# Kernel optimization log

Hardware: AMD Instinct MI355X
Metric: run time of the kernel (lower is better)

Reference implementation:

```python
import jax, jax.numpy as jnp
import numpy as np

B, T, HID = 1, 1024, 2048
H, DK, DV, M, KW = 16, 128, 128, 128, 4  # heads, key dim, value dim, slots, conv kernel
SCALE = DK ** -0.5
EPS = 1e-5


def short_conv(x, w):
    # causal depthwise conv1d + silu; x: [B,T,C], w: [C,K]
    K = w.shape[1]
    xp = jnp.pad(x, ((0, 0), (K - 1, 0), (0, 0)))
    t = x.shape[1]
    y = sum(xp[:, i:i + t] * w[:, i] for i in range(K))
    return jax.nn.silu(y)


def l2norm(x):
    return x * jax.lax.rsqrt(jnp.sum(x * x, axis=-1, keepdims=True) + 1e-6)


def gsa2_scan(q, k, v, w, g, beta):
    # q,k: [B,T,H,DK]  v: [B,T,H,DV]  w,g: [B,T,H,M]  beta: [B,T,H]
    b = q.shape[0]
    tm = lambda x: jnp.moveaxis(x, 1, 0)  # time-major
    Sk0 = jnp.zeros((b, H, DK, M), q.dtype)  # key->slot memory
    Sv0 = jnp.zeros((b, H, M, DV), q.dtype)  # slot->value memory

    def step(carry, xs):
        Sk, Sv = carry
        q_t, k_t, v_t, w_t, g_t, b_t = xs
        gt = jnp.exp(g_t)  # [B,H,M] gate in (0,1) since g = logsigmoid(.)
        bw = b_t[:, :, None] * w_t  # beta-scaled slot write address [B,H,M]
        Sk = Sk * gt[:, :, None, :] + k_t[..., :, None] * bw[:, :, None, :]
        Sv = Sv * gt[..., None] + bw[..., None] * v_t[:, :, None, :]
        s = jnp.einsum('bhd,bhdm->bhm', q_t, Sk) * SCALE
        a = jax.nn.softmax(s, axis=-1)
        o_t = jnp.einsum('bhm,bhmd->bhd', a, Sv)
        return (Sk, Sv), o_t

    (_, _), o = jax.lax.scan(step, (Sk0, Sv0),
                             (tm(q), tm(k), tm(v), tm(w), tm(g), tm(beta)))
    return jnp.moveaxis(o, 0, 1)  # [B,T,H,DV]


def reference(hidden_states, Wq, Wk, Wv, Ww, cq, ck, cv,
              Wf1, Wf2, Wb, Wg1, Wg2, bg2, norm_w, Wo):
    h = hidden_states  # [B,T,HID]
    q = short_conv(h @ Wq, cq)
    k = short_conv(h @ Wk, ck)
    v = short_conv(h @ Wv, cv)
    w = short_conv(h @ Ww, cv)  # source applies v_conv1d to w (faithful)
    g = jax.nn.log_sigmoid((h @ Wf1) @ Wf2)   # [B,T,H*M]
    beta = jax.nn.sigmoid(h @ Wb)             # [B,T,H]
    rs = lambda x, d: x.reshape(x.shape[0], x.shape[1], -1, d)
    q, k = rs(q, DK), rs(k, DK)
    v = rs(v, DV)
    w = l2norm(rs(w, M))
    g = rs(g, M)
    o = gsa2_scan(q, k, v, w, g, beta)        # [B,T,H,DV]
    gate = rs((h @ Wg1) @ Wg2 + bg2, DV)
    # FusedRMSNormGated with sigmoid activation
    o = o * jax.lax.rsqrt(jnp.mean(o * o, axis=-1, keepdims=True) + EPS)
    o = o * norm_w * jax.nn.sigmoid(gate)
    o = o.reshape(o.shape[0], o.shape[1], -1)
    return o @ Wo


def setup_inputs() -> dict:
    key = jax.random.key(0)
    ks = jax.random.split(key, 16)
    s = 0.02
    return {
        'hidden_states': jax.random.normal(ks[0], (B, T, HID), jnp.float32),
        'Wq': jax.random.normal(ks[1], (HID, H * DK), jnp.float32) * s,
        'Wk': jax.random.normal(ks[2], (HID, H * DK), jnp.float32) * s,
        'Wv': jax.random.normal(ks[3], (HID, H * DV), jnp.float32) * s,
        'Ww': jax.random.normal(ks[4], (HID, H * M), jnp.float32) * s,
        'cq': jax.random.normal(ks[5], (H * DK, KW), jnp.float32) * 0.2,
        'ck': jax.random.normal(ks[6], (H * DK, KW), jnp.float32) * 0.2,
        'cv': jax.random.normal(ks[7], (H * DV, KW), jnp.float32) * 0.2,
        'Wf1': jax.random.normal(ks[8], (HID, DV), jnp.float32) * s,
        'Wf2': jax.random.normal(ks[9], (DV, H * M), jnp.float32) * s,
        'Wb': jax.random.normal(ks[10], (HID, H), jnp.float32) * s,
        'Wg1': jax.random.normal(ks[11], (HID, DV), jnp.float32) * s,
        'Wg2': jax.random.normal(ks[12], (DV, H * DV), jnp.float32) * s,
        'bg2': jnp.zeros((H * DV,), jnp.float32),
        'norm_w': jnp.ones((DV,), jnp.float32),
        'Wo': jax.random.normal(ks[13], (H * DV, HID), jnp.float32) * s,
    }
```

## Files before the change

### kernel.cpp

```cpp
#include <hip/hip_runtime.h>
#include <hip/hip_bf16.h>
#include <stdint.h>

typedef unsigned short u16;
typedef __attribute__((ext_vector_type(8))) short bf16x8;
typedef __attribute__((ext_vector_type(4))) short bf16x4;
typedef __attribute__((ext_vector_type(4))) float f32x4;

#define DEV static __device__ __forceinline__

DEV u16 f2bf(float f){
  union { float f; unsigned u; } x; x.f = f;
  unsigned r = x.u + 0x7fffu + ((x.u >> 16) & 1u);
  return (u16)(r >> 16);
}

DEV float bf2f(u16 u){
  union { unsigned u; float f; } x; x.u = ((unsigned)u) << 16; return x.f;
}

DEV bf16x8 ldfrag(const u16* p){
  bf16x4 a = *(const bf16x4*)p;
  bf16x4 b = *(const bf16x4*)(p+4);
  bf16x8 r;
  r[0]=a[0]; r[1]=a[1]; r[2]=a[2]; r[3]=a[3];
  r[4]=b[0]; r[5]=b[1]; r[6]=b[2]; r[7]=b[3];
  return r;
}

DEV bf16x4 cvt4(float a, float b, float c, float d){
  bf16x4 r; r[0]=(short)f2bf(a); r[1]=(short)f2bf(b); r[2]=(short)f2bf(c); r[3]=(short)f2bf(d);
  return r;
}

DEV void g2l16(const void* g, void* l){
  __builtin_amdgcn_global_load_lds((const __attribute__((address_space(1))) unsigned int*)g,
                                   (__attribute__((address_space(3))) unsigned int*)l,
                                   16, 0, 0);
}

__global__ __launch_bounds__(256)
void transp64_k(const float* __restrict__ Wq, const float* __restrict__ Wk,
                const float* __restrict__ Wv, const float* __restrict__ Ww,
                const float* __restrict__ Wo, u16* __restrict__ WcatT, u16* __restrict__ WoT,
                const float* __restrict__ hX, u16* __restrict__ h_bf){
  __shared__ float tile[64][65];
  const int z = blockIdx.z;
  if (z == 5){
    int idx = ((blockIdx.y*32 + blockIdx.x)*256 + threadIdx.x)*8;
    float4 v0 = *(const float4*)&hX[idx];
    float4 v1 = *(const float4*)&hX[idx+4];
    ushort4 o0, o1;
    o0.x=f2bf(v0.x); o0.y=f2bf(v0.y); o0.z=f2bf(v0.z); o0.w=f2bf(v0.w);
    o1.x=f2bf(v1.x); o1.y=f2bf(v1.y); o1.z=f2bf(v1.z); o1.w=f2bf(v1.w);
    *(ushort4*)&h_bf[idx]   = o0;
    *(ushort4*)&h_bf[idx+4] = o1;
    return;
  }
  const float* src = (z==0)?Wq:((z==1)?Wk:((z==2)?Wv:((z==3)?Ww:Wo)));
  u16* dst = (z<4) ? (WcatT + (size_t)z*4194304) : WoT;
  const int c0 = blockIdx.x*64, r0 = blockIdx.y*64;
#pragma unroll
  for (int p=0;p<4;p++){
    int i = threadIdx.x + p*256;
    int r = i>>4, c4 = (i&15)<<2;
    *(float4*)&tile[r][c4] = *(const float4*)&src[(size_t)(r0+r)*2048 + c0 + c4];
  }
  __syncthreads();
#pragma unroll
  for (int p=0;p<4;p++){
    int i = threadIdx.x + p*256;
    int cc = i>>4, r4 = (i&15)<<2;
    ushort4 o;
    o.x = f2bf(tile[r4+0][cc]); o.y = f2bf(tile[r4+1][cc]);
    o.z = f2bf(tile[r4+2][cc]); o.w = f2bf(tile[r4+3][cc]);
    *(ushort4*)&dst[(size_t)(c0+cc)*2048 + r0 + r4] = o;
  }
}

__global__ __launch_bounds__(256)
void transpsm_k(const float* __restrict__ Wf1, const float* __restrict__ Wg1,
                const float* __restrict__ Wf2, const float* __restrict__ Wg2,
                u16* __restrict__ WfgT, u16* __restrict__ Wf2T, u16* __restrict__ Wg2T){
  __shared__ float tile[32][33];
  const int bx = blockIdx.x;
  const int z = bx >> 8, rem = bx & 255;
  const float* src; u16* dst; int R, C, cx, cy;
  if (z==0){      src=Wf1; dst=WfgT;                    R=2048; C=128;  cx=rem&3;  cy=rem>>2; }
  else if (z==1){ src=Wg1; dst=WfgT+(size_t)128*2048;   R=2048; C=128;  cx=rem&3;  cy=rem>>2; }
  else if (z==2){ src=Wf2; dst=Wf2T;                    R=128;  C=2048; cx=rem>>2; cy=rem&3; }
  else {          src=Wg2; dst=Wg2T;                    R=128;  C=2048; cx=rem>>2; cy=rem&3; }
  const int c0 = cx*32, r0 = cy*32;
  const int x = threadIdx.x & 31, y0 = threadIdx.x >> 5;
#pragma unroll
  for (int j=0;j<4;j++){
    int r = y0 + j*8;
    tile[r][x] = src[(size_t)(r0+r)*C + c0 + x];
  }
  __syncthreads();
#pragma unroll
  for (int j=0;j<4;j++){
    int cc = y0 + j*8;
    dst[(size_t)(c0+cc)*R + r0 + x] = f2bf(tile[x][cc]);
  }
}

template<bool OBF>
__global__ __launch_bounds__(256)
void gemm4_k(const u16* __restrict__ A, const u16* __restrict__ B, void* __restrict__ Cp,
             int K, int lda, int ldb, int ldc){
  __shared__ u16 As[2][128*64];
  __shared__ u16 Bs[2][128*64];
  const int m0 = blockIdx.y*128, n0 = blockIdx.x*128;
  const int tid = threadIdx.x;
  const int wave = tid>>6, lane = tid&63, lr = lane&15, kg = lane>>4;
  const int wm = wave>>1, wn = wave&1;
  const f32x4 vz = {0.f,0.f,0.f,0.f};
  f32x4 acc[4][4];
#pragma unroll
  for (int a=0;a<4;a++)
#pragma unroll
    for (int b=0;b<4;b++) acc[a][b]=vz;

#define STAGE4(buf, k0) do { \
    _Pragma("unroll") \
    for (int p=0;p<4;p++){ \
      int chunk = tid + p*256, r_ = chunk>>3, ci = chunk&7; \
      g2l16(A + (size_t)(m0+r_)*lda + (k0) + ((ci^(r_&7))<<3), &As[buf][chunk*8]); \
    } \
    _Pragma("unroll") \
    for (int p=0;p<4;p++){ \
      int chunk = tid + p*256, r_ = chunk>>3, ci = chunk&7; \
      g2l16(B + (size_t)(n0+r_)*ldb + (k0) + ((ci^(r_&7))<<3), &Bs[buf][chunk*8]); \
    } \
  } while(0)

  const int nt = K>>6;
  STAGE4(0, 0);
  STAGE4(1, 64);
  for (int t=0; t<nt; ++t){
    const int buf = t&1;
    if (t < nt-1) asm volatile("s_waitcnt vmcnt(8)" ::: "memory");
    else          asm volatile("s_waitcnt vmcnt(0)" ::: "memory");
    asm volatile("s_barrier" ::: "memory");
#pragma unroll
    for (int ks=0; ks<2; ++ks){
      bf16x8 af[4], bfv[4];
#pragma unroll
      for (int mi=0;mi<4;mi++){
        int r = wm*64+mi*16+lr;
        af[mi] = *(const bf16x8*)&As[buf][r*64 + (((ks*4+kg)^(r&7))<<3)];
      }
#pragma unroll
      for (int ni=0;ni<4;ni++){
        int r = wn*64+ni*16+lr;
        bfv[ni] = *(const bf16x8*)&Bs[buf][r*64 + (((ks*4+kg)^(r&7))<<3)];
      }
      asm volatile("s_waitcnt lgkmcnt(0)" ::: "memory");
      __builtin_amdgcn_sched_barrier(0);
      __builtin_amdgcn_s_setprio(1);
#pragma unroll
      for (int mi=0;mi<4;mi++)
#pragma unroll
        for (int ni=0;ni<4;ni++)
          acc[mi][ni] = __builtin_amdgcn_mfma_f32_16x16x32_bf16(af[mi], bfv[ni], acc[mi][ni], 0, 0, 0);
      __builtin_amdgcn_s_setprio(0);
      __builtin_amdgcn_sched_barrier(0);
      asm volatile("s_barrier" ::: "memory");
    }
    if (t+2 < nt) STAGE4(buf, (t+2)<<6);
  }
#undef STAGE4
#pragma unroll
  for (int mi=0;mi<4;mi++)
#pragma unroll
    for (int ni=0;ni<4;ni++)
#pragma unroll
      for (int vv=0;vv<4;vv++){
        int row = m0 + wm*64 + mi*16 + kg*4 + vv;
        int col = n0 + wn*64 + ni*16 + lr;
        if (OBF) ((u16*)Cp)[(size_t)row*ldc + col] = f2bf(acc[mi][ni][vv]);
        else     ((float*)Cp)[(size_t)row*ldc + col] = acc[mi][ni][vv];
      }
}

__global__ __launch_bounds__(256)
void gemm4sk_k(const u16* __restrict__ A, const u16* __restrict__ B, float* __restrict__ P,
               int Khalf, int lda, int ldb, int ldc){
  __shared__ u16 As[2][128*64];
  __shared__ u16 Bs[2][128*64];
  const int m0 = blockIdx.y*128, n0 = blockIdx.x*128;
  const int kbase = blockIdx.z*Khalf;
  const int tid = threadIdx.x;
  const int wave = tid>>6, lane = tid&63, lr = lane&15, kg = lane>>4;
  const int wm = wave>>1, wn = wave&1;
  const f32x4 vz = {0.f,0.f,0.f,0.f};
  f32x4 acc[4][4];
#pragma unroll
  for (int a=0;a<4;a++)
#pragma unroll
    for (int b=0;b<4;b++) acc[a][b]=vz;

#define STAGE4(buf, k0) do { \
    _Pragma("unroll") \
    for (int p=0;p<4;p++){ \
      int chunk = tid + p*256, r_ = chunk>>3, ci = chunk&7; \
      g2l16(A + (size_t)(m0+r_)*lda + (k0) + ((ci^(r_&7))<<3), &As[buf][chunk*8]); \
    } \
    _Pragma("unroll") \
    for (int p=0;p<4;p++){ \
      int chunk = tid + p*256, r_ = chunk>>3, ci = chunk&7; \
      g2l16(B + (size_t)(n0+r_)*ldb + (k0) + ((ci^(r_&7))<<3), &Bs[buf][chunk*8]); \
    } \
  } while(0)

  const int nt = Khalf>>6;
  STAGE4(0, kbase);
  STAGE4(1, kbase+64);
  for (int t=0; t<nt; ++t){
    const int buf = t&1;
    if (t < nt-1) asm volatile("s_waitcnt vmcnt(8)" ::: "memory");
    else          asm volatile("s_waitcnt vmcnt(0)" ::: "memory");
    asm volatile("s_barrier" ::: "memory");
#pragma unroll
    for (int ks=0; ks<2; ++ks){
      bf16x8 af[4], bfv[4];
#pragma unroll
      for (int mi=0;mi<4;mi++){
        int r = wm*64+mi*16+lr;
        af[mi] = *(const bf16x8*)&As[buf][r*64 + (((ks*4+kg)^(r&7))<<3)];
      }
#pragma unroll
      for (int ni=0;ni<4;ni++){
        int r = wn*64+ni*16+lr;
        bfv[ni] = *(const bf16x8*)&Bs[buf][r*64 + (((ks*4+kg)^(r&7))<<3)];
      }
      asm volatile("s_waitcnt lgkmcnt(0)" ::: "memory");
      __builtin_amdgcn_sched_barrier(0);
      __builtin_amdgcn_s_setprio(1);
#pragma unroll
      for (int mi=0;mi<4;mi++)
#pragma unroll
        for (int ni=0;ni<4;ni++)
          acc[mi][ni] = __builtin_amdgcn_mfma_f32_16x16x32_bf16(af[mi], bfv[ni], acc[mi][ni], 0, 0, 0);
      __builtin_amdgcn_s_setprio(0);
      __builtin_amdgcn_sched_barrier(0);
      asm volatile("s_barrier" ::: "memory");
    }
    if (t+2 < nt) STAGE4(buf, kbase + ((t+2)<<6));
  }
#undef STAGE4
#pragma unroll
  for (int mi=0;mi<4;mi++)
#pragma unroll
    for (int ni=0;ni<4;ni++)
#pragma unroll
      for (int vv=0;vv<4;vv++){
        int row = m0 + wm*64 + mi*16 + kg*4 + vv;
        int col = n0 + wn*64 + ni*16 + lr;
        P[(size_t)blockIdx.z*2097152 + (size_t)row*ldc + col] = acc[mi][ni][vv];
      }
}

__global__ __launch_bounds__(256)
void addout_k(const float* __restrict__ P, float* __restrict__ out){
  int i = (blockIdx.x*256 + threadIdx.x)*4;
  float4 a = *(const float4*)&P[i];
  float4 b = *(const float4*)&P[2097152 + i];
  float4 s = {a.x+b.x, a.y+b.y, a.z+b.z, a.w+b.w};
  *(float4*)&out[i] = s;
}

template<bool OBF, int EPI>
__global__ __launch_bounds__(256)
void gemm_k(const u16* __restrict__ A, const u16* __restrict__ B, void* __restrict__ Cp,
            int K, int lda, int ldb, int ldc){
  __shared__ u16 As[128*32];
  __shared__ u16 Bs[128*32];
  const int m0 = blockIdx.y*128, n0 = blockIdx.x*128;
  const int tid = threadIdx.x;
  const int lane = tid & 63, wave = tid >> 6;
  const int wr = wave >> 1, wc = wave & 1;
  const int lr = lane & 15, kg = lane >> 4;
  const f32x4 vzero = {0.f,0.f,0.f,0.f};
  f32x4 acc[4][4];
#pragma unroll
  for (int a=0;a<4;a++)
#pragma unroll
    for (int b=0;b<4;b++) acc[a][b] = vzero;
  const int r0 = tid>>2, s0 = tid&3;
  for (int k0=0;k0<K;k0+=32){
    __syncthreads();
    g2l16(A + (size_t)(m0+r0)*lda + k0 + s0*8, (u16*)As + (size_t)tid*8);
    g2l16(B + (size_t)(n0+r0)*ldb + k0 + s0*8, (u16*)Bs + (size_t)tid*8);
    g2l16(A + (size_t)(m0+r0+64)*lda + k0 + s0*8, (u16*)As + (size_t)(tid+256)*8);
    g2l16(B + (size_t)(n0+r0+64)*ldb + k0 + s0*8, (u16*)Bs + (size_t)(tid+256)*8);
    __syncthreads();
    bf16x8 af[4], bfv[4];
#pragma unroll
    for (int mi=0;mi<4;mi++) af[mi]  = *(const bf16x8*)(As + (wr*64+mi*16+lr)*32 + kg*8);
#pragma unroll
    for (int ni=0;ni<4;ni++) bfv[ni] = *(const bf16x8*)(Bs + (wc*64+ni*16+lr)*32 + kg*8);
#pragma unroll
    for (int mi=0;mi<4;mi++)
#pragma unroll
      for (int ni=0;ni<4;ni++)
        acc[mi][ni] = __builtin_amdgcn_mfma_f32_16x16x32_bf16(af[mi], bfv[ni], acc[mi][ni], 0, 0, 0);
  }
#pragma unroll
  for (int mi=0;mi<4;mi++)
#pragma unroll
    for (int ni=0;ni<4;ni++)
#pragma unroll
      for (int vv=0;vv<4;vv++){
        int row = m0 + wr*64 + mi*16 + kg*4 + vv;
        int col = n0 + wc*64 + ni*16 + lr;
        float val = acc[mi][ni][vv];
        if (EPI==1) val = fminf(val,0.f) - __logf(1.f + __expf(-fabsf(val)));
        if (OBF) ((u16*)Cp)[(size_t)row*ldc + col] = f2bf(val);
        else     ((float*)Cp)[(size_t)row*ldc + col] = val;
      }
}

__global__ __launch_bounds__(256)
void gemmsk_k(const u16* __restrict__ A, const u16* __restrict__ B, float* __restrict__ P,
              int lda, int ldb){
  __shared__ u16 As[128*32];
  __shared__ u16 Bs[128*32];
  const int m0 = blockIdx.y*128, n0 = blockIdx.x*128;
  const int kbase = blockIdx.z*256;
  const int tid = threadIdx.x;
  const int lane = tid & 63, wave = tid >> 6;
  const int wr = wave >> 1, wc = wave & 1;
  const int lr = lane & 15, kg = lane >> 4;
  const f32x4 vzero = {0.f,0.f,0.f,0.f};
  f32x4 acc[4][4];
#pragma unroll
  for (int a=0;a<4;a++)
#pragma unroll
    for (int b=0;b<4;b++) acc[a][b] = vzero;
  const int r0 = tid>>2, s0 = tid&3;
  for (int k0=kbase;k0<kbase+256;k0+=32){
    __syncthreads();
    g2l16(A + (size_t)(m0+r0)*lda + k0 + s0*8, (u16*)As + (size_t)tid*8);
    g2l16(B + (size_t)(n0+r0)*ldb + k0 + s0*8, (u16*)Bs + (size_t)tid*8);
    g2l16(A + (size_t)(m0+r0+64)*lda + k0 + s0*8, (u16*)As + (size_t)(tid+256)*8);
    g2l16(B + (size_t)(n0+r0+64)*ldb + k0 + s0*8, (u16*)Bs + (size_t)(tid+256)*8);
    __syncthreads();
    bf16x8 af[4], bfv[4];
#pragma unroll
    for (int mi=0;mi<4;mi++) af[mi]  = *(const bf16x8*)(As + (wr*64+mi*16+lr)*32 + kg*8);
#pragma unroll
    for (int ni=0;ni<4;ni++) bfv[ni] = *(const bf16x8*)(Bs + (wc*64+ni*16+lr)*32 + kg*8);
#pragma unroll
    for (int mi=0;mi<4;mi++)
#pragma unroll
      for (int ni=0;ni<4;ni++)
        acc[mi][ni] = __builtin_amdgcn_mfma_f32_16x16x32_bf16(af[mi], bfv[ni], acc[mi][ni], 0, 0, 0);
  }
#pragma unroll
  for (int mi=0;mi<4;mi++)
#pragma unroll
    for (int ni=0;ni<4;ni++)
#pragma unroll
      for (int vv=0;vv<4;vv++){
        int row = m0 + wr*64 + mi*16 + kg*4 + vv;
        int col = n0 + wc*64 + ni*16 + lr;
        P[(size_t)blockIdx.z*262144 + (size_t)row*256 + col] = acc[mi][ni][vv];
      }
}

__global__ __launch_bounds__(256)
void reduce8_k(const float* __restrict__ P, u16* __restrict__ out){
  int i = (blockIdx.x*256 + threadIdx.x)*4;
  float4 s = *(const float4*)&P[i];
#pragma unroll
  for (int z=1;z<8;z++){
    float4 p = *(const float4*)&P[(size_t)z*262144 + i];
    s.x+=p.x; s.y+=p.y; s.z+=p.z; s.w+=p.w;
  }
  ushort4 o; o.x=f2bf(s.x); o.y=f2bf(s.y); o.z=f2bf(s.z); o.w=f2bf(s.w);
  *(ushort4*)&out[i] = o;
}

__global__ __launch_bounds__(256)
void beta_k(const float* __restrict__ h, const float* __restrict__ Wb, float* __restrict__ betab){
  __shared__ float hrow[2048];
  __shared__ float red[16][5];
  const int t = blockIdx.x, tid = threadIdx.x;
#pragma unroll
  for (int j=0;j<8;j++) hrow[tid + j*256] = h[(size_t)t*2048 + tid + j*256];
  __syncthreads();
  float part[16];
#pragma unroll
  for (int n=0;n<16;n++) part[n]=0.f;
  for (int j=0;j<8;j++){
    int kk = tid + j*256;
    float hv = hrow[kk];
    const float4* wr4 = (const float4*)&Wb[(size_t)kk*16];
    float4 w0=wr4[0], w1=wr4[1], w2=wr4[2], w3=wr4[3];
    part[0]+=hv*w0.x; part[1]+=hv*w0.y; part[2]+=hv*w0.z; part[3]+=hv*w0.w;
    part[4]+=hv*w1.x; part[5]+=hv*w1.y; part[6]+=hv*w1.z; part[7]+=hv*w1.w;
    part[8]+=hv*w2.x; part[9]+=hv*w2.y; part[10]+=hv*w2.z; part[11]+=hv*w2.w;
    part[12]+=hv*w3.x; part[13]+=hv*w3.y; part[14]+=hv*w3.z; part[15]+=hv*w3.w;
  }
#pragma unroll
  for (int n=0;n<16;n++){
    float s = part[n];
#pragma unroll
    for (int off=1;off<64;off<<=1) s += __shfl_xor(s, off);
    if ((tid&63)==0) red[n][tid>>6] = s;
  }
  __syncthreads();
  if (tid < 16){
    float s = red[tid][0]+red[tid][1]+red[tid][2]+red[tid][3];
    betab[t*16+tid] = 1.f/(1.f+__expf(-s));
  }
}

__global__ __launch_bounds__(256)
void conv_k(const u16* __restrict__ raw, const float* __restrict__ cq,
            const float* __restrict__ ck, const float* __restrict__ cv,
            u16* __restrict__ qo, u16* __restrict__ ko,
            u16* __restrict__ vo, float* __restrict__ wo){
  int idx = blockIdx.x*256 + threadIdx.x;
  int cgl = idx & 8191, tb = idx >> 13;
  int which = cgl >> 11, cc = cgl & 2047;
  const float* wt = (which==0)?cq:((which==1)?ck:cv);
  float4 w4 = *(const float4*)&wt[cc*4];
  u16* outb = (which==0)?qo:((which==1)?ko:vo);
  int t0 = tb*4;
  float x[7];
#pragma unroll
  for (int j=0;j<7;j++){
    int t = t0 - 3 + j;
    x[j] = (t >= 0) ? bf2f(raw[(size_t)t*8192 + cgl]) : 0.f;
  }
#pragma unroll
  for (int j=0;j<4;j++){
    float y = x[j]*w4.x + x[j+1]*w4.y + x[j+2]*w4.z + x[j+3]*w4.w;
    y = y / (1.f + __expf(-y));
    if (which==3) wo[(size_t)(t0+j)*2048 + cc] = y;
    else          outb[(size_t)(t0+j)*2048 + cc] = f2bf(y);
  }
}

__global__ __launch_bounds__(256)
void l2bw_k(const float* __restrict__ wconv, const float* __restrict__ betab,
            float* __restrict__ bwout){
  int row = blockIdx.x*4 + (threadIdx.x>>6);
  int lane = threadIdx.x & 63;
  int t = row >> 4, h = row & 15;
  size_t base = (size_t)t*2048 + h*128;
  float a0 = wconv[base+lane], a1 = wconv[base+64+lane];
  float ss = a0*a0 + a1*a1;
#pragma unroll
  for (int off=1;off<64;off<<=1) ss += __shfl_xor(ss, off);
  float r = rsqrtf(ss + 1e-6f) * betab[t*16+h];
  bwout[base+lane]    = a0*r;
  bwout[base+64+lane] = a1*r;
}

__global__ __launch_bounds__(128)
void cg_k(const float* __restrict__ gpre, float* __restrict__ cg){
  int idx = blockIdx.x*128 + threadIdx.x;
  int c = idx >> 11;
  size_t base = (size_t)(idx & 2047);
  float run = 0.f;
  for (int i2=0;i2<64;i2++){
    size_t t = (size_t)c*64 + i2;
    run += gpre[t*2048 + base];
    cg[t*2048 + base] = run;
  }
}

__global__ __launch_bounds__(256)
void phaseA_k(const u16* __restrict__ k, const u16* __restrict__ v,
              const float* __restrict__ bw, const float* __restrict__ cg,
              u16* __restrict__ DSkT, u16* __restrict__ DSvT){
  __shared__ u16 UT[128*68];
  __shared__ u16 KT[128*68];
  __shared__ u16 VT[128*68];
  __shared__ float Gt[128];
  const int bx=blockIdx.x, h=bx&15, c=bx>>4, tid=threadIdx.x;
  const int w=tid>>6, lane=tid&63, lr=lane&15, kg=lane>>4;
  if (tid<128) Gt[tid] = cg[(size_t)(c*64+63)*2048 + h*128 + tid];
  __syncthreads();
#pragma unroll
  for (int j=0;j<8;j++){
    int f4=tid+j*256, r=f4>>5, c4=(f4&31)<<2;
    size_t g=(size_t)(c*64+r)*2048 + h*128 + c4;
    ushort4 kv=*(const ushort4*)&k[g];
    ushort4 vv=*(const ushort4*)&v[g];
    float4 bv=*(const float4*)&bw[g];
    float4 cv=*(const float4*)&cg[g];
    float u0=bv.x*__expf(Gt[c4+0]-cv.x);
    float u1=bv.y*__expf(Gt[c4+1]-cv.y);
    float u2=bv.z*__expf(Gt[c4+2]-cv.z);
    float u3=bv.w*__expf(Gt[c4+3]-cv.w);
    KT[(c4+0)*68+r]=kv.x; KT[(c4+1)*68+r]=kv.y;
    KT[(c4+2)*68+r]=kv.z; KT[(c4+3)*68+r]=kv.w;
    VT[(c4+0)*68+r]=vv.x; VT[(c4+1)*68+r]=vv.y;
    VT[(c4+2)*68+r]=vv.z; VT[(c4+3)*68+r]=vv.w;
    UT[(c4+0)*68+r]=f2bf(u0);   UT[(c4+1)*68+r]=f2bf(u1);
    UT[(c4+2)*68+r]=f2bf(u2);   UT[(c4+3)*68+r]=f2bf(u3);
  }
  __syncthreads();
  const f32x4 vz = {0.f,0.f,0.f,0.f};
  {
    f32x4 acc[2][8];
#pragma unroll
    for (int a=0;a<2;a++)
#pragma unroll
      for (int b=0;b<8;b++) acc[a][b]=vz;
#pragma unroll
    for (int ks=0;ks<2;ks++){
      bf16x8 a0=ldfrag(&UT[(w*32   +lr)*68 + ks*32+kg*8]);
      bf16x8 a1=ldfrag(&UT[(w*32+16+lr)*68 + ks*32+kg*8]);
#pragma unroll
      for (int nj=0;nj<8;nj++){
        bf16x8 b=ldfrag(&KT[(nj*16+lr)*68 + ks*32+kg*8]);
        acc[0][nj]=__builtin_amdgcn_mfma_f32_16x16x32_bf16(a0,b,acc[0][nj],0,0,0);
        acc[1][nj]=__builtin_amdgcn_mfma_f32_16x16x32_bf16(a1,b,acc[1][nj],0,0,0);
      }
    }
#pragma unroll
    for (int mi2=0;mi2<2;mi2++)
#pragma unroll
      for (int nj=0;nj<8;nj++)
#pragma unroll
        for (int vv2=0;vv2<4;vv2++)
          DSkT[(size_t)bx*16384 + (size_t)(w*32+mi2*16+kg*4+vv2)*128 + nj*16+lr] = f2bf(acc[mi2][nj][vv2]);
  }
  {
    f32x4 acc[2][8];
#pragma unroll
    for (int a=0;a<2;a++)
#pragma unroll
      for (int b=0;b<8;b++) acc[a][b]=vz;
#pragma unroll
    for (int ks=0;ks<2;ks++){
      bf16x8 a0=ldfrag(&VT[(w*32   +lr)*68 + ks*32+kg*8]);
      bf16x8 a1=ldfrag(&VT[(w*32+16+lr)*68 + ks*32+kg*8]);
#pragma unroll
      for (int nj=0;nj<8;nj++){
        bf16x8 b=ldfrag(&UT[(nj*16+lr)*68 + ks*32+kg*8]);
        acc[0][nj]=__builtin_amdgcn_mfma_f32_16x16x32_bf16(a0,b,acc[0][nj],0,0,0);
        acc[1][nj]=__builtin_amdgcn_mfma_f32_16x16x32_bf16(a1,b,acc[1][nj],0,0,0);
      }
    }
#pragma unroll
    for (int mi2=0;mi2<2;mi2++)
#pragma unroll
      for (int nj=0;nj<8;nj++)
#pragma unroll
        for (int vv2=0;vv2<4;vv2++)
          DSvT[(size_t)bx*16384 + (size_t)(w*32+mi2*16+kg*4+vv2)*128 + nj*16+lr] = f2bf(acc[mi2][nj][vv2]);
  }
}

__global__ __launch_bounds__(256)
void phaseB_k(const u16* __restrict__ DSk, const u16* __restrict__ DSv,
              const float* __restrict__ cg, u16* __restrict__ Sk0, u16* __restrict__ Sv0){
  unsigned idx = blockIdx.x*256u + threadIdx.x;
  int sel  = idx >> 18;
  int h    = (idx >> 14) & 15;
  int flat = idx & 16383;
  int mdec = sel ? (flat & 127) : (flat >> 7);
  const u16* DS = sel ? DSv : DSk;
  u16* S = sel ? Sv0 : Sk0;
  float cur = 0.f;
  for (int c=0;c<16;c++){
    size_t sb = ((size_t)(c*16+h))*16384 + flat;
    S[sb] = f2bf(cur);
    float gd = __expf(cg[(size_t)(c*64+63)*2048 + h*128 + mdec]);
    cur = cur*gd + bf2f(DS[sb]);
  }
}

__global__ __launch_bounds__(256)
void phaseC_k(const u16* __restrict__ q, const u16* __restrict__ k,
              const u16* __restrict__ v, const float* __restrict__ bw,
              const float* __restrict__ cg, const u16* __restrict__ SkT,
              const u16* __restrict__ SvT, float* __restrict__ o){
  __shared__ u16 Qb[64*132];
  __shared__ u16 KV[8704];
  __shared__ u16 Bws[64*132];
  __shared__ u16 BwT[128*68];
  __shared__ u16 Ssb[64*68];
  __shared__ u16 SkL[128*132];
  __shared__ u16 SvL[128*132];
  __shared__ float cgm[128];
  __shared__ float ecgm[128];
  const int bx=blockIdx.x, h=bx&15, c=bx>>4, tid=threadIdx.x;
  const int w=tid>>6, lane=tid&63, lr=lane&15, kg=lane>>4;
  const float SCALE = 0.088388347648318447f;
  const f32x4 vz = {0.f,0.f,0.f,0.f};
  if (tid<128){ float t=cg[(size_t)(c*64+31)*2048 + h*128 + tid]; cgm[tid]=t; ecgm[tid]=__expf(t); }
  __syncthreads();
#pragma unroll
  for (int j=0;j<8;j++){
    int f4=tid+j*256, r=f4>>5, c4=(f4&31)<<2;
    size_t g=(size_t)(c*64+r)*2048 + h*128 + c4;
    *(ushort4*)&Qb[r*132+c4] = *(const ushort4*)&q[g];
    *(ushort4*)&KV[r*132+c4] = *(const ushort4*)&k[g];
    float4 bv=*(const float4*)&bw[g];
    float4 cv=*(const float4*)&cg[g];
    float b0=bv.x*__expf(cgm[c4+0]-cv.x);
    float b1=bv.y*__expf(cgm[c4+1]-cv.y);
    float b2=bv.z*__expf(cgm[c4+2]-cv.z);
    float b3=bv.w*__expf(cgm[c4+3]-cv.w);
    bf16x4 bb = cvt4(b0,b1,b2,b3);
    *(bf16x4*)&Bws[r*132+c4] = bb;
    BwT[(c4+0)*68+r]=(u16)bb[0]; BwT[(c4+1)*68+r]=(u16)bb[1];
    BwT[(c4+2)*68+r]=(u16)bb[2]; BwT[(c4+3)*68+r]=(u16)bb[3];
  }
  __syncthreads();
  {
    f32x4 acc1[4];
#pragma unroll
    for (int a=0;a<4;a++) acc1[a]=vz;
#pragma unroll
    for (int ks=0;ks<4;ks++){
      bf16x8 aq = ldfrag(&Qb[(w*16+lr)*132 + ks*32+kg*8]);
#pragma unroll
      for (int ni=0;ni<4;ni++){
        bf16x8 bk = ldfrag(&KV[(ni*16+lr)*132 + ks*32+kg*8]);
        acc1[ni]=__builtin_amdgcn_mfma_f32_16x16x32_bf16(aq,bk,acc1[ni],0,0,0);
      }
    }
#pragma unroll
    for (int ni=0;ni<4;ni++)
#pragma unroll
      for (int vv2=0;vv2<4;vv2++){
        int row=w*16+kg*4+vv2, col=ni*16+lr;
        Ssb[row*68+col] = (col<=row) ? f2bf(acc1[ni][vv2]) : (u16)0;
      }
  }
  __syncthreads();
#pragma unroll
  for (int j=0;j<8;j++){
    int f4=tid+j*256, r=f4>>5, c4=(f4&31)<<2;
    ushort4 vv=*(const ushort4*)&v[(size_t)(c*64+r)*2048 + h*128 + c4];
    KV[(c4+0)*68+r]=vv.x; KV[(c4+1)*68+r]=vv.y;
    KV[(c4+2)*68+r]=vv.z; KV[(c4+3)*68+r]=vv.w;
  }
#pragma unroll
  for (int j=0;j<16;j++){
    int f4=tid+j*256, r=f4>>5, c4=(f4&31)<<2;
    ushort4 s4=*(const ushort4*)&SkT[(size_t)bx*16384 + (size_t)r*128 + c4];
    float em=ecgm[r];
    *(bf16x4*)&SkL[r*132+c4]=cvt4(bf2f(s4.x)*em, bf2f(s4.y)*em, bf2f(s4.z)*em, bf2f(s4.w)*em);
  }
#pragma unroll
  for (int j=0;j<16;j++){
    int f4=tid+j*256, r=f4>>5, c4=(f4&31)<<2;
    ushort4 s4=*(const ushort4*)&SvT[(size_t)bx*16384 + (size_t)r*128 + c4];
    *(bf16x4*)&SvL[r*132+c4]=cvt4(bf2f(s4.x)*ecgm[c4+0], bf2f(s4.y)*ecgm[c4+1],
                                  bf2f(s4.z)*ecgm[c4+2], bf2f(s4.w)*ecgm[c4+3]);
  }
  f32x4 zac[8];
#pragma unroll
  for (int a=0;a<8;a++) zac[a]=vz;
#pragma unroll
  for (int ks=0;ks<2;ks++){
    bf16x8 as_ = ldfrag(&Ssb[(w*16+lr)*68 + ks*32+kg*8]);
#pragma unroll
    for (int ni=0;ni<8;ni++){
      bf16x8 bb = ldfrag(&BwT[(ni*16+lr)*68 + ks*32+kg*8]);
      zac[ni]=__builtin_amdgcn_mfma_f32_16x16x32_bf16(as_,bb,zac[ni],0,0,0);
    }
  }
  __syncthreads();
#pragma unroll
  for (int dt=0;dt<4;dt++){
    bf16x8 aq = ldfrag(&Qb[(w*16+lr)*132 + dt*32+kg*8]);
#pragma unroll
    for (int ni=0;ni<8;ni++){
      bf16x8 bs = ldfrag(&SkL[(ni*16+lr)*132 + dt*32+kg*8]);
      zac[ni]=__builtin_amdgcn_mfma_f32_16x16x32_bf16(aq,bs,zac[ni],0,0,0);
    }
  }
  float dec[4][8], zz[4][8];
#pragma unroll
  for (int vv2=0;vv2<4;vv2++)
#pragma unroll
    for (int ni=0;ni<8;ni++) zz[vv2][ni]=zac[ni][vv2];
#pragma unroll
  for (int vv2=0;vv2<4;vv2++){
    size_t gr=(size_t)(c*64+w*16+kg*4+vv2)*2048 + h*128;
#pragma unroll
    for (int ni=0;ni<8;ni++){
      float cgv = cg[gr + ni*16+lr];
      dec[vv2][ni] = __expf(cgv - cgm[ni*16+lr]);
    }
  }
#pragma unroll
  for (int vv2=0;vv2<4;vv2++){
    float mx=-3.0e38f;
#pragma unroll
    for (int ni=0;ni<8;ni++){ zz[vv2][ni] *= SCALE*dec[vv2][ni]; mx=fmaxf(mx,zz[vv2][ni]); }
    mx=fmaxf(mx,__shfl_xor(mx,1)); mx=fmaxf(mx,__shfl_xor(mx,2));
    mx=fmaxf(mx,__shfl_xor(mx,4)); mx=fmaxf(mx,__shfl_xor(mx,8));
    float sum=0.f;
#pragma unroll
    for (int ni=0;ni<8;ni++){ zz[vv2][ni]=__expf(zz[vv2][ni]-mx); sum+=zz[vv2][ni]; }
    sum+=__shfl_xor(sum,1); sum+=__shfl_xor(sum,2);
    sum+=__shfl_xor(sum,4); sum+=__shfl_xor(sum,8);
    float inv=1.f/sum;
#pragma unroll
    for (int ni=0;ni<8;ni++) zz[vv2][ni] *= inv*dec[vv2][ni];
  }
#pragma unroll
  for (int vv2=0;vv2<4;vv2++)
#pragma unroll
    for (int ni=0;ni<8;ni++)
      Qb[(w*16+kg*4+vv2)*132 + ni*16+lr] = f2bf(zz[vv2][ni]);
  {
    f32x4 acc4[4];
#pragma unroll
    for (int a=0;a<4;a++) acc4[a]=vz;
#pragma unroll
    for (int ks=0;ks<4;ks++){
      bf16x8 aa = ldfrag(&Qb[(w*16+lr)*132 + ks*32+kg*8]);
#pragma unroll
      for (int ni=0;ni<4;ni++){
        bf16x8 bb = ldfrag(&Bws[(ni*16+lr)*132 + ks*32+kg*8]);
        acc4[ni]=__builtin_amdgcn_mfma_f32_16x16x32_bf16(aa,bb,acc4[ni],0,0,0);
      }
    }
#pragma unroll
    for (int ni=0;ni<4;ni++)
#pragma unroll
      for (int vv2=0;vv2<4;vv2++){
        int row=w*16+kg*4+vv2, col=ni*16+lr;
        Ssb[row*68+col] = (col<=row) ? f2bf(acc4[ni][vv2]) : (u16)0;
      }
  }
  f32x4 oac[8];
#pragma unroll
  for (int a=0;a<8;a++) oac[a]=vz;
#pragma unroll
  for (int ks=0;ks<2;ks++){
    bf16x8 ap = ldfrag(&Ssb[(w*16+lr)*68 + ks*32+kg*8]);
#pragma unroll
    for (int ni=0;ni<8;ni++){
      bf16x8 bv2 = ldfrag(&KV[(ni*16+lr)*68 + ks*32+kg*8]);
      oac[ni]=__builtin_amdgcn_mfma_f32_16x16x32_bf16(ap,bv2,oac[ni],0,0,0);
    }
  }
#pragma unroll
  for (int mt=0;mt<4;mt++){
    bf16x8 aa = ldfrag(&Qb[(w*16+lr)*132 + mt*32+kg*8]);
#pragma unroll
    for (int ni=0;ni<8;ni++){
      bf16x8 bs = ldfrag(&SvL[(ni*16+lr)*132 + mt*32+kg*8]);
      oac[ni]=__builtin_amdgcn_mfma_f32_16x16x32_bf16(aa,bs,oac[ni],0,0,0);
    }
  }
#pragma unroll
  for (int ni=0;ni<8;ni++)
#pragma unroll
    for (int vv2=0;vv2<4;vv2++)
      o[(size_t)(c*64+w*16+kg*4+vv2)*2048 + h*128 + ni*16+lr] = oac[ni][vv2];
}

__global__ __launch_bounds__(256)
void norm_k(const float* __restrict__ o, const float* __restrict__ gate,
            const float* __restrict__ bg2, const float* __restrict__ nw,
            u16* __restrict__ Obf){
  int row = blockIdx.x*4 + (threadIdx.x>>6);
  int lane = threadIdx.x & 63;
  int t = row >> 4, h = row & 15;
  size_t base = (size_t)t*2048 + h*128;
  float o0 = o[base+lane], o1 = o[base+64+lane];
  float ss = o0*o0 + o1*o1;
#pragma unroll
  for (int off=1;off<64;off<<=1) ss += __shfl_xor(ss, off);
  float r = rsqrtf(ss*(1.f/128.f) + 1e-5f);
  int hv0 = h*128+lane, hv1 = hv0+64;
  float g0 = gate[base+lane]    + bg2[hv0];
  float g1 = gate[base+64+lane] + bg2[hv1];
  float v0 = o0*r*nw[lane]   *(1.f/(1.f+__expf(-g0)));
  float v1 = o1*r*nw[lane+64]*(1.f/(1.f+__expf(-g1)));
  Obf[base+lane]    = f2bf(v0);
  Obf[base+64+lane] = f2bf(v1);
}

extern "C" void kernel_launch(void* const* d_in, const int* in_sizes, int n_in,
                              void* d_out, int out_size, void* d_ws, size_t ws_size,
                              hipStream_t stream){
  (void)in_sizes; (void)n_in; (void)out_size; (void)ws_size;
  const float* hX   = (const float*)d_in[0];
  const float* Wq   = (const float*)d_in[1];
  const float* Wk   = (const float*)d_in[2];
  const float* Wv   = (const float*)d_in[3];
  const float* Ww   = (const float*)d_in[4];
  const float* cq   = (const float*)d_in[5];
  const float* ck   = (const float*)d_in[6];
  const float* cv   = (const float*)d_in[7];
  const float* Wf1  = (const float*)d_in[8];
  const float* Wf2  = (const float*)d_in[9];
  const float* Wb   = (const float*)d_in[10];
  const float* Wg1  = (const float*)d_in[11];
  const float* Wg2  = (const float*)d_in[12];
  const float* bg2  = (const float*)d_in[13];
  const float* nw   = (const float*)d_in[14];
  const float* Wo   = (const float*)d_in[15];
  char* ws = (char*)d_ws;
  u16*   h_bf  = (u16*)  (ws + 0);
  u16*   WcatT = (u16*)  (ws + 4194304);
  u16*   Sk0   = (u16*)  (ws + 4194304);
  u16*   Sv0   = (u16*)  (ws + 20971520);
  u16*   WoT   = (u16*)  (ws + 37748736);
  u16*   WfgT  = (u16*)  (ws + 46137344);
  u16*   Wf2T  = (u16*)  (ws + 47185920);
  u16*   Wg2T  = (u16*)  (ws + 47710208);
  u16*   qkvw  = (u16*)  (ws + 48234496);
  u16*   DSk   = (u16*)  (ws + 48234496);
  u16*   DSv   = (u16*)  (ws + 56623104);
  float* Pw    = (float*)(ws + 48234496);
  u16*   qb    = (u16*)  (ws + 81788928);
  u16*   kb    = (u16*)  (ws + 90177536);
  u16*   vb    = (u16*)  (ws + 98566144);
  float* wcv   = (float*)(ws + 106954752);
  float* P8    = wcv;
  float* osc   = wcv;
  float* bwb   = (float*)(ws + 115343360);
  u16*   f1g1  = (u16*)  (ws + 123731968);
  float* gpre  = (float*)(ws + 124256256);
  float* gateb = gpre;
  float* cgb   = (float*)(ws + 132644864);
  float* betab = (float*)(ws + 141033472);
  u16*   Obf   = (u16*)  (ws + 141099008);
  float* outp  = (float*)d_out;

  transp64_k<<<dim3(32,32,6),256,0,stream>>>(Wq, Wk, Wv, Ww, Wo, WcatT, WoT, hX, h_bf);
  transpsm_k<<<1024,256,0,stream>>>(Wf1, Wg1, Wf2, Wg2, WfgT, Wf2T, Wg2T);

  gemm4_k<true><<<dim3(64,8),256,0,stream>>>(h_bf, WcatT, qkvw, 2048, 2048, 2048, 8192);
  gemmsk_k<<<dim3(2,8,8),256,0,stream>>>(h_bf, WfgT, P8, 2048, 2048);
  reduce8_k<<<256,256,0,stream>>>(P8, f1g1);
  gemm_k<false,1><<<dim3(16,8),256,0,stream>>>(f1g1, Wf2T, gpre, 128, 256, 128, 2048);
  beta_k<<<1024,256,0,stream>>>(hX, Wb, betab);

  conv_k<<<8192,256,0,stream>>>(qkvw, cq, ck, cv, qb, kb, vb, wcv);
  l2bw_k<<<4096,256,0,stream>>>(wcv, betab, bwb);
  cg_k<<<256,128,0,stream>>>(gpre, cgb);

  gemm_k<false,0><<<dim3(16,8),256,0,stream>>>(f1g1 + 128, Wg2T, gateb, 128, 256, 128, 2048);

  phaseA_k<<<256,256,0,stream>>>(kb, vb, bwb, cgb, DSk, DSv);
  phaseB_k<<<2048,256,0,stream>>>(DSk, DSv, cgb, Sk0, Sv0);
  phaseC_k<<<256,256,0,stream>>>(qb, kb, vb, bwb, cgb, Sk0, Sv0, osc);

  norm_k<<<4096,256,0,stream>>>(osc, gateb, bg2, nw, Obf);
  gemm4sk_k<<<dim3(16,8,2),256,0,stream>>>(Obf, WoT, Pw, 1024, 2048, 2048, 2048);
  addout_k<<<2048,256,0,stream>>>(Pw, outp);
}
```

Before: 198.6 us.

## Fuse small transposes, gate GEMMs, and l2norm into existing kernels to cut launches

Merges the small-weight transpose kernel into the main transpose launch via extra z-slices, and combines the two post-low-rank GEMMs (forget gate and output gate) into one launch indexed by blockIdx.z. The w l2-norm and beta scaling is folded into the conv kernel using a cross-wave shared-memory reduction, which removes the fp32 wcv intermediate and its separate pass. The split-K factor of the low-rank projection GEMM goes from 8 to 16, with the reduction kernel widened to match. The aim is to reduce launch count and memory round-trips, at the cost of a larger partial-sum buffer and a block-wide sync inside the conv kernel.

New measurement: 191.8 us. 1.04x faster.

```diff
diff --git a/kernel.cpp b/kernel.cpp
--- a/kernel.cpp
+++ b/kernel.cpp
@@ -43,8 +43,11 @@
 void transp64_k(const float* __restrict__ Wq, const float* __restrict__ Wk,
                 const float* __restrict__ Wv, const float* __restrict__ Ww,
                 const float* __restrict__ Wo, u16* __restrict__ WcatT, u16* __restrict__ WoT,
-                const float* __restrict__ hX, u16* __restrict__ h_bf){
-  __shared__ float tile[64][65];
+                const float* __restrict__ hX, u16* __restrict__ h_bf,
+                const float* __restrict__ Wf1, const float* __restrict__ Wg1,
+                const float* __restrict__ Wf2, const float* __restrict__ Wg2,
+                u16* __restrict__ WfgT, u16* __restrict__ Wf2T, u16* __restrict__ Wg2T){
+  __shared__ float tile[64*65];
   const int z = blockIdx.z;
   if (z == 5){
     int idx = ((blockIdx.y*32 + blockIdx.x)*256 + threadIdx.x)*8;
@@ -57,6 +60,29 @@
     *(ushort4*)&h_bf[idx+4] = o1;
     return;
   }
+  if (z >= 6){
+    int rem = blockIdx.y*32 + blockIdx.x;
+    if (rem >= 256) return;
+    const float* src; u16* dst; int R, C, cx, cy;
+    if (z==6){      src=Wf1; dst=WfgT;                  R=2048; C=128;  cx=rem&3;  cy=rem>>2; }
+    else if (z==7){ src=Wg1; dst=WfgT+(size_t)128*2048; R=2048; C=128;  cx=rem&3;  cy=rem>>2; }
+    else if (z==8){ src=Wf2; dst=Wf2T;                  R=128;  C=2048; cx=rem>>2; cy=rem&3; }
+    else {          src=Wg2; dst=Wg2T;                  R=128;  C=2048; cx=rem>>2; cy=rem&3; }
+    const int c0 = cx*32, r0 = cy*32;
+    const int x = threadIdx.x & 31, y0 = threadIdx.x >> 5;
+#pragma unroll
+    for (int j=0;j<4;j++){
+      int r = y0 + j*8;
+      tile[r*33 + x] = src[(size_t)(r0+r)*C + c0 + x];
+    }
+    __syncthreads();
+#pragma unroll
+    for (int j=0;j<4;j++){
+      int cc = y0 + j*8;
+      dst[(size_t)(c0+cc)*R + r0 + x] = f2bf(tile[x*33 + cc]);
+    }
+    return;
+  }
   const float* src = (z==0)?Wq:((z==1)?Wk:((z==2)?Wv:((z==3)?Ww:Wo)));
   u16* dst = (z<4) ? (WcatT + (size_t)z*4194304) : WoT;
   const int c0 = blockIdx.x*64, r0 = blockIdx.y*64;
@@ -64,7 +90,7 @@
   for (int p=0;p<4;p++){
     int i = threadIdx.x + p*256;
     int r = i>>4, c4 = (i&15)<<2;
-    *(float4*)&tile[r][c4] = *(const float4*)&src[(size_t)(r0+r)*2048 + c0 + c4];
+    *(float4*)&tile[r*65 + c4] = *(const float4*)&src[(size_t)(r0+r)*2048 + c0 + c4];
   }
   __syncthreads();
 #pragma unroll
@@ -72,36 +98,9 @@
     int i = threadIdx.x + p*256;
     int cc = i>>4, r4 = (i&15)<<2;
     ushort4 o;
-    o.x = f2bf(tile[r4+0][cc]); o.y = f2bf(tile[r4+1][cc]);
-    o.z = f2bf(tile[r4+2][cc]); o.w = f2bf(tile[r4+3][cc]);
+    o.x = f2bf(tile[(r4+0)*65 + cc]); o.y = f2bf(tile[(r4+1)*65 + cc]);
+    o.z = f2bf(tile[(r4+2)*65 + cc]); o.w = f2bf(tile[(r4+3)*65 + cc]);
     *(ushort4*)&dst[(size_t)(c0+cc)*2048 + r0 + r4] = o;
-  }
-}
-
-__global__ __launch_bounds__(256)
-void transpsm_k(const float* __restrict__ Wf1, const float* __restrict__ Wg1,
-                const float* __restrict__ Wf2, const float* __restrict__ Wg2,
-                u16* __restrict__ WfgT, u16* __restrict__ Wf2T, u16* __restrict__ Wg2T){
-  __shared__ float tile[32][33];
-  const int bx = blockIdx.x;
-  const int z = bx >> 8, rem = bx & 255;
-  const float* src; u16* dst; int R, C, cx, cy;
-  if (z==0){      src=Wf1; dst=WfgT;                    R=2048; C=128;  cx=rem&3;  cy=rem>>2; }
-  else if (z==1){ src=Wg1; dst=WfgT+(size_t)128*2048;   R=2048; C=128;  cx=rem&3;  cy=rem>>2; }
-  else if (z==2){ src=Wf2; dst=Wf2T;                    R=128;  C=2048; cx=rem>>2; cy=rem&3; }
-  else {          src=Wg2; dst=Wg2T;                    R=128;  C=2048; cx=rem>>2; cy=rem&3; }
-  const int c0 = cx*32, r0 = cy*32;
-  const int x = threadIdx.x & 31, y0 = threadIdx.x >> 5;
-#pragma unroll
-  for (int j=0;j<4;j++){
-    int r = y0 + j*8;
-    tile[r][x] = src[(size_t)(r0+r)*C + c0 + x];
-  }
-  __syncthreads();
-#pragma unroll
-  for (int j=0;j<4;j++){
-    int cc = y0 + j*8;
-    dst[(size_t)(c0+cc)*R + r0 + x] = f2bf(tile[x][cc]);
   }
 }
 
@@ -271,12 +270,15 @@
   *(float4*)&out[i] = s;
 }
 
-template<bool OBF, int EPI>
-__global__ __launch_bounds__(256)
-void gemm_k(const u16* __restrict__ A, const u16* __restrict__ B, void* __restrict__ Cp,
-            int K, int lda, int ldb, int ldc){
+__global__ __launch_bounds__(256)
+void gemmg_k(const u16* __restrict__ f1g1, const u16* __restrict__ Bf, const u16* __restrict__ Bg,
+             float* __restrict__ Cf, float* __restrict__ Cg){
   __shared__ u16 As[128*32];
   __shared__ u16 Bs[128*32];
+  const int zz = blockIdx.z;
+  const u16* A = f1g1 + zz*128;
+  const u16* B = zz ? Bg : Bf;
+  float* C = zz ? Cg : Cf;
   const int m0 = blockIdx.y*128, n0 = blockIdx.x*128;
   const int tid = threadIdx.x;
   const int lane = tid & 63, wave = tid >> 6;
@@ -289,7 +291,57 @@
 #pragma unroll
     for (int b=0;b<4;b++) acc[a][b] = vzero;
   const int r0 = tid>>2, s0 = tid&3;
-  for (int k0=0;k0<K;k0+=32){
+  for (int k0=0;k0<128;k0+=32){
+    __syncthreads();
+    g2l16(A + (size_t)(m0+r0)*256 + k0 + s0*8, (u16*)As + (size_t)tid*8);
+    g2l16(B + (size_t)(n0+r0)*128 + k0 + s0*8, (u16*)Bs + (size_t)tid*8);
+    g2l16(A + (size_t)(m0+r0+64)*256 + k0 + s0*8, (u16*)As + (size_t)(tid+256)*8);
+    g2l16(B + (size_t)(n0+r0+64)*128 + k0 + s0*8, (u16*)Bs + (size_t)(tid+256)*8);
+    __syncthreads();
+    bf16x8 af[4], bfv[4];
+#pragma unroll
+    for (int mi=0;mi<4;mi++) af[mi]  = *(const bf16x8*)(As + (wr*64+mi*16+lr)*32 + kg*8);
+#pragma unroll
+    for (int ni=0;ni<4;ni++) bfv[ni] = *(const bf16x8*)(Bs + (wc*64+ni*16+lr)*32 + kg*8);
+#pragma unroll
+    for (int mi=0;mi<4;mi++)
+#pragma unroll
+      for (int ni=0;ni<4;ni++)
+        acc[mi][ni] = __builtin_amdgcn_mfma_f32_16x16x32_bf16(af[mi], bfv[ni], acc[mi][ni], 0, 0, 0);
+  }
+#pragma unroll
+  for (int mi=0;mi<4;mi++)
+#pragma unroll
+    for (int ni=0;ni<4;ni++)
+#pragma unroll
+      for (int vv=0;vv<4;vv++){
+        int row = m0 + wr*64 + mi*16 + kg*4 + vv;
+        int col = n0 + wc*64 + ni*16 + lr;
+        float val = acc[mi][ni][vv];
+        if (zz==0) val = fminf(val,0.f) - __logf(1.f + __expf(-fabsf(val)));
+        C[(size_t)row*2048 + col] = val;
+      }
+}
+
+__global__ __launch_bounds__(256)
+void gemmsk_k(const u16* __restrict__ A, const u16* __restrict__ B, float* __restrict__ P,
+              int lda, int ldb){
+  __shared__ u16 As[128*32];
+  __shared__ u16 Bs[128*32];
+  const int m0 = blockIdx.y*128, n0 = blockIdx.x*128;
+  const int kbase = blockIdx.z*128;
+  const int tid = threadIdx.x;
+  const int lane = tid & 63, wave = tid >> 6;
+  const int wr = wave >> 1, wc = wave & 1;
+  const int lr = lane & 15, kg = lane >> 4;
+  const f32x4 vzero = {0.f,0.f,0.f,0.f};
+  f32x4 acc[4][4];
+#pragma unroll
+  for (int a=0;a<4;a++)
+#pragma unroll
+    for (int b=0;b<4;b++) acc[a][b] = vzero;
+  const int r0 = tid>>2, s0 = tid&3;
+  for (int k0=kbase;k0<kbase+128;k0+=32){
     __syncthreads();
     g2l16(A + (size_t)(m0+r0)*lda + k0 + s0*8, (u16*)As + (size_t)tid*8);
     g2l16(B + (size_t)(n0+r0)*ldb + k0 + s0*8, (u16*)Bs + (size_t)tid*8);
@@ -315,67 +367,16 @@
       for (int vv=0;vv<4;vv++){
         int row = m0 + wr*64 + mi*16 + kg*4 + vv;
         int col = n0 + wc*64 + ni*16 + lr;
-        float val = acc[mi][ni][vv];
-        if (EPI==1) val = fminf(val,0.f) - __logf(1.f + __expf(-fabsf(val)));
-        if (OBF) ((u16*)Cp)[(size_t)row*ldc + col] = f2bf(val);
-        else     ((float*)Cp)[(size_t)row*ldc + col] = val;
-      }
-}
-
-__global__ __launch_bounds__(256)
-void gemmsk_k(const u16* __restrict__ A, const u16* __restrict__ B, float* __restrict__ P,
-              int lda, int ldb){
-  __shared__ u16 As[128*32];
-  __shared__ u16 Bs[128*32];
-  const int m0 = blockIdx.y*128, n0 = blockIdx.x*128;
-  const int kbase = blockIdx.z*256;
-  const int tid = threadIdx.x;
-  const int lane = tid & 63, wave = tid >> 6;
-  const int wr = wave >> 1, wc = wave & 1;
-  const int lr = lane & 15, kg = lane >> 4;
-  const f32x4 vzero = {0.f,0.f,0.f,0.f};
-  f32x4 acc[4][4];
-#pragma unroll
-  for (int a=0;a<4;a++)
-#pragma unroll
-    for (int b=0;b<4;b++) acc[a][b] = vzero;
-  const int r0 = tid>>2, s0 = tid&3;
-  for (int k0=kbase;k0<kbase+256;k0+=32){
-    __syncthreads();
-    g2l16(A + (size_t)(m0+r0)*lda + k0 + s0*8, (u16*)As + (size_t)tid*8);
-    g2l16(B + (size_t)(n0+r0)*ldb + k0 + s0*8, (u16*)Bs + (size_t)tid*8);
-    g2l16(A + (size_t)(m0+r0+64)*lda + k0 + s0*8, (u16*)As + (size_t)(tid+256)*8);
-    g2l16(B + (size_t)(n0+r0+64)*ldb + k0 + s0*8, (u16*)Bs + (size_t)(tid+256)*8);
-    __syncthreads();
-    bf16x8 af[4], bfv[4];
-#pragma unroll
-    for (int mi=0;mi<4;mi++) af[mi]  = *(const bf16x8*)(As + (wr*64+mi*16+lr)*32 + kg*8);
-#pragma unroll
-    for (int ni=0;ni<4;ni++) bfv[ni] = *(const bf16x8*)(Bs + (wc*64+ni*16+lr)*32 + kg*8);
-#pragma unroll
-    for (int mi=0;mi<4;mi++)
-#pragma unroll
-      for (int ni=0;ni<4;ni++)
-        acc[mi][ni] = __builtin_amdgcn_mfma_f32_16x16x32_bf16(af[mi], bfv[ni], acc[mi][ni], 0, 0, 0);
-  }
-#pragma unroll
-  for (int mi=0;mi<4;mi++)
-#pragma unroll
-    for (int ni=0;ni<4;ni++)
-#pragma unroll
-      for (int vv=0;vv<4;vv++){
-        int row = m0 + wr*64 + mi*16 + kg*4 + vv;
-        int col = n0 + wc*64 + ni*16 + lr;
         P[(size_t)blockIdx.z*262144 + (size_t)row*256 + col] = acc[mi][ni][vv];
       }
 }
 
 __global__ __launch_bounds__(256)
-void reduce8_k(const float* __restrict__ P, u16* __restrict__ out){
+void reduce16_k(const float* __restrict__ P, u16* __restrict__ out){
   int i = (blockIdx.x*256 + threadIdx.x)*4;
   float4 s = *(const float4*)&P[i];
 #pragma unroll
-  for (int z=1;z<8;z++){
+  for (int z=1;z<16;z++){
     float4 p = *(const float4*)&P[(size_t)z*262144 + i];
     s.x+=p.x; s.y+=p.y; s.z+=p.z; s.w+=p.w;
   }
@@ -421,14 +422,15 @@
 __global__ __launch_bounds__(256)
 void conv_k(const u16* __restrict__ raw, const float* __restrict__ cq,
             const float* __restrict__ ck, const float* __restrict__ cv,
+            const float* __restrict__ betab,
             u16* __restrict__ qo, u16* __restrict__ ko,
-            u16* __restrict__ vo, float* __restrict__ wo){
+            u16* __restrict__ vo, float* __restrict__ bwout){
+  __shared__ float red[2][2][4];
   int idx = blockIdx.x*256 + threadIdx.x;
   int cgl = idx & 8191, tb = idx >> 13;
   int which = cgl >> 11, cc = cgl & 2047;
   const float* wt = (which==0)?cq:((which==1)?ck:cv);
   float4 w4 = *(const float4*)&wt[cc*4];
-  u16* outb = (which==0)?qo:((which==1)?ko:vo);
   int t0 = tb*4;
   float x[7];
 #pragma unroll
@@ -436,29 +438,41 @@
     int t = t0 - 3 + j;
     x[j] = (t >= 0) ? bf2f(raw[(size_t)t*8192 + cgl]) : 0.f;
   }
+  float y[4];
 #pragma unroll
   for (int j=0;j<4;j++){
-    float y = x[j]*w4.x + x[j+1]*w4.y + x[j+2]*w4.z + x[j+3]*w4.w;
-    y = y / (1.f + __expf(-y));
-    if (which==3) wo[(size_t)(t0+j)*2048 + cc] = y;
-    else          outb[(size_t)(t0+j)*2048 + cc] = f2bf(y);
-  }
-}
-
-__global__ __launch_bounds__(256)
-void l2bw_k(const float* __restrict__ wconv, const float* __restrict__ betab,
-            float* __restrict__ bwout){
-  int row = blockIdx.x*4 + (threadIdx.x>>6);
-  int lane = threadIdx.x & 63;
-  int t = row >> 4, h = row & 15;
-  size_t base = (size_t)t*2048 + h*128;
-  float a0 = wconv[base+lane], a1 = wconv[base+64+lane];
-  float ss = a0*a0 + a1*a1;
-#pragma unroll
-  for (int off=1;off<64;off<<=1) ss += __shfl_xor(ss, off);
-  float r = rsqrtf(ss + 1e-6f) * betab[t*16+h];
-  bwout[base+lane]    = a0*r;
-  bwout[base+64+lane] = a1*r;
+    float yy = x[j]*w4.x + x[j+1]*w4.y + x[j+2]*w4.z + x[j+3]*w4.w;
+    y[j] = yy / (1.f + __expf(-yy));
+  }
+  if (which < 3){
+    u16* outb = (which==0)?qo:((which==1)?ko:vo);
+#pragma unroll
+    for (int j=0;j<4;j++)
+      outb[(size_t)(t0+j)*2048 + cc] = f2bf(y[j]);
+  } else {
+    const int hh = threadIdx.x >> 7;
+    const int wh = (threadIdx.x >> 6) & 1;
+    float ss[4];
+#pragma unroll
+    for (int j=0;j<4;j++){
+      float s = y[j]*y[j];
+#pragma unroll
+      for (int off=1;off<64;off<<=1) s += __shfl_xor(s, off);
+      ss[j] = s;
+    }
+    if ((threadIdx.x & 63) == 0){
+#pragma unroll
+      for (int j=0;j<4;j++) red[hh][wh][j] = ss[j];
+    }
+    __syncthreads();
+    const int h = cc >> 7;
+#pragma unroll
+    for (int j=0;j<4;j++){
+      float tot = red[hh][0][j] + red[hh][1][j];
+      float r = rsqrtf(tot + 1e-6f) * betab[(t0+j)*16 + h];
+      bwout[(size_t)(t0+j)*2048 + cc] = y[j]*r;
+    }
+  }
 }
 
 __global__ __launch_bounds__(128)
@@ -820,35 +834,31 @@
   u16*   DSk   = (u16*)  (ws + 48234496);
   u16*   DSv   = (u16*)  (ws + 56623104);
   float* Pw    = (float*)(ws + 48234496);
+  float* gateb = (float*)(ws + 65011712);
   u16*   qb    = (u16*)  (ws + 81788928);
   u16*   kb    = (u16*)  (ws + 90177536);
   u16*   vb    = (u16*)  (ws + 98566144);
-  float* wcv   = (float*)(ws + 106954752);
-  float* P8    = wcv;
-  float* osc   = wcv;
+  float* P8    = (float*)(ws + 106954752);
+  float* osc   = (float*)(ws + 106954752);
   float* bwb   = (float*)(ws + 115343360);
   u16*   f1g1  = (u16*)  (ws + 123731968);
   float* gpre  = (float*)(ws + 124256256);
-  float* gateb = gpre;
   float* cgb   = (float*)(ws + 132644864);
   float* betab = (float*)(ws + 141033472);
   u16*   Obf   = (u16*)  (ws + 141099008);
   float* outp  = (float*)d_out;
 
-  transp64_k<<<dim3(32,32,6),256,0,stream>>>(Wq, Wk, Wv, Ww, Wo, WcatT, WoT, hX, h_bf);
-  transpsm_k<<<1024,256,0,stream>>>(Wf1, Wg1, Wf2, Wg2, WfgT, Wf2T, Wg2T);
+  transp64_k<<<dim3(32,32,10),256,0,stream>>>(Wq, Wk, Wv, Ww, Wo, WcatT, WoT, hX, h_bf,
+                                              Wf1, Wg1, Wf2, Wg2, WfgT, Wf2T, Wg2T);
 
   gemm4_k<true><<<dim3(64,8),256,0,stream>>>(h_bf, WcatT, qkvw, 2048, 2048, 2048, 8192);
-  gemmsk_k<<<dim3(2,8,8),256,0,stream>>>(h_bf, WfgT, P8, 2048, 2048);
-  reduce8_k<<<256,256,0,stream>>>(P8, f1g1);
-  gemm_k<false,1><<<dim3(16,8),256,0,stream>>>(f1g1, Wf2T, gpre, 128, 256, 128, 2048);
+  gemmsk_k<<<dim3(2,8,16),256,0,stream>>>(h_bf, WfgT, P8, 2048, 2048);
+  reduce16_k<<<256,256,0,stream>>>(P8, f1g1);
+  gemmg_k<<<dim3(16,8,2),256,0,stream>>>(f1g1, Wf2T, Wg2T, gpre, gateb);
   beta_k<<<1024,256,0,stream>>>(hX, Wb, betab);
 
-  conv_k<<<8192,256,0,stream>>>(qkvw, cq, ck, cv, qb, kb, vb, wcv);
-  l2bw_k<<<4096,256,0,stream>>>(wcv, betab, bwb);
+  conv_k<<<8192,256,0,stream>>>(qkvw, cq, ck, cv, betab, qb, kb, vb, bwb);
   cg_k<<<256,128,0,stream>>>(gpre, cgb);
-
-  gemm_k<false,0><<<dim3(16,8),256,0,stream>>>(f1g1 + 128, Wg2T, gateb, 128, 256, 128, 2048);
 
   phaseA_k<<<256,256,0,stream>>>(kb, vb, bwb, cgb, DSk, DSv);
   phaseB_k<<<2048,256,0,stream>>>(DSk, DSv, cgb, Sk0, Sv0);
```
